# Kernel tuning notes

Hardware: AMD Instinct MI355X
Metric: run time of the kernel (lower is better)

Reference implementation:

```python
import jax, jax.numpy as jnp
import numpy as np

CDIM = 32
SCALES = (1, 16, 64, 256, 1024, 4096)  # last entry == T
INV_TEMP = 100.0
ENT_W = 0.1
COMMIT_W = 0.2
Q_SCALE = 1.0 / float(np.sqrt(CDIM))


def _interp_area(x, pt):
    # x: [B, T, C] -> [B, pt, C]; T divisible by pt so 'area' == block mean
    B, T, C = x.shape
    return x.reshape(B, pt, T // pt, C).mean(axis=2)


def _interp_linear(x, T):
    # x: [B, pt, C] -> [B, T, C]; mode='linear', align_corners=False
    pt = x.shape[1]
    pos = (jnp.arange(T, dtype=jnp.float32) + 0.5) * (pt / T) - 0.5
    pos = jnp.clip(pos, 0.0, pt - 1.0)
    lo = jnp.floor(pos).astype(jnp.int32)
    hi = jnp.minimum(lo + 1, pt - 1)
    w = (pos - lo.astype(jnp.float32))[None, :, None]
    return x[:, lo] * (1.0 - w) + x[:, hi] * w


def _bsq(f):
    # L2 normalize (torch F.normalize: clamp_min on norm)
    f = f / jnp.maximum(jnp.linalg.norm(f, axis=-1, keepdims=True), 1e-12)
    # sign quantize with STE
    zhat = jnp.where(f > 0, Q_SCALE, -Q_SCALE).astype(f.dtype)
    quantized = f + jax.lax.stop_gradient(zhat - f)
    # soft entropy loss
    p = jax.nn.sigmoid(-4.0 * f * (INV_TEMP / float(np.sqrt(CDIM))))
    prob = jnp.stack([p, 1.0 - p], axis=-1)  # [B, T, C, 2]
    ent = lambda c: -(c * jnp.log(c + 1e-8)).sum(axis=-1)
    per_sample_entropy = ent(prob).sum(axis=-1).mean()
    avg_prob = prob.mean(axis=(0, 1))  # [C, 2]
    cb_entropy = ent(avg_prob).sum()
    entropy_penalty = (per_sample_entropy - cb_entropy) / INV_TEMP
    commit = ((jax.lax.stop_gradient(quantized) - f) ** 2).sum(axis=-1).mean()
    aux = entropy_penalty * ENT_W + commit * COMMIT_W
    bits = (quantized > 0).astype(jnp.int32)
    return quantized, bits, aux


def setup_inputs() -> dict:
    key = jax.random.key(0)
    B, T, C = 128, SCALES[-1], CDIM
    return {"f_BTC": jax.random.normal(key, (B, T, C), dtype=jnp.float32)}


def reference(f_BTC):
    B, T, C = f_BTC.shape
    quantized_out = jnp.zeros_like(f_BTC)
    residual = f_BTC
    losses, bit_list = [], []
    for pt in SCALES:
        interp_res = _interp_area(residual, pt) if pt != T else residual
        q, bits, loss = _bsq(interp_res)
        q = _interp_linear(q, T) if pt != T else q
        residual = residual - jax.lax.stop_gradient(q)
        quantized_out = quantized_out + q
        bit_list.append(bits)
        losses.append(loss)
    all_losses = jnp.stack(losses, axis=-1)       # [num_scales]
    all_bits = jnp.concatenate(bit_list, axis=1)  # [B, sum(SCALES), C]
    return quantized_out, all_bits, all_losses
```

## Files before the change

kernel.cpp:

```cpp
#include <hip/hip_runtime.h>
#include <hip/hip_bf16.h>
#include <cstddef>
#include <cstdint>

#define NB 128
#define NT 4096
#define NC 32
#define BITROWS 5457
#define QV_ROWS 1361
#define QOUT_ELEMS (NB*NT*NC)
#define BITS_ELEMS (NB*BITROWS*NC)

#define ACC_OFF  22298624
#define S16_OFF  22302720

__device__ __constant__ float kQSC = 0.17677669529663687f;
__device__ __constant__ float kSIG = 17.67766952966369f;

__device__ __forceinline__ float interp_eval(const float* __restrict__ q, int P, int t, int c) {
  float pos = ((float)t + 0.5f) * ((float)P * (1.0f / 4096.0f)) - 0.5f;
  pos = fminf(fmaxf(pos, 0.0f), (float)(P - 1));
  const int lo = (int)pos;
  const int hi = min(lo + 1, P - 1);
  const float w = pos - (float)lo;
  const float a = __fmul_rn(q[lo * NC + c], 1.0f - w);
  const float b = __fmul_rn(q[hi * NC + c], w);
  return __fadd_rn(a, b);
}

__device__ __forceinline__ float interp_slice(const float* __restrict__ q, int P, int base, int t, int c) {
  float pos = ((float)t + 0.5f) * ((float)P * (1.0f / 4096.0f)) - 0.5f;
  pos = fminf(fmaxf(pos, 0.0f), (float)(P - 1));
  const int lo = (int)pos;
  const int hi = min(lo + 1, P - 1);
  const float w = pos - (float)lo;
  const float a = __fmul_rn(q[(lo - base) * NC + c], 1.0f - w);
  const float b = __fmul_rn(q[(hi - base) * NC + c], w);
  return __fadd_rn(a, b);
}

__device__ __forceinline__ void process_elem(
    float msum, float invn, int b, int rowOff, int j, int c,
    float* qlsRow, float* __restrict__ qvG, float* __restrict__ bitsG,
    float& entA, float& comA, float& pA)
{
  const float m = msum * invn;
  float ss = m * m;
  #pragma unroll
  for (int mk = 16; mk; mk >>= 1) ss += __shfl_xor(ss, mk, 32);
  const float den = fmaxf(sqrtf(ss), 1e-12f);
  const float fn = m / den;
  const bool bit = fn > 0.0f;
  const float zh = bit ? kQSC : -kQSC;
  const float qvv = fn + (zh - fn);
  if (qlsRow) qlsRow[c] = qvv;
  if (qvG) qvG[(size_t)b * (QV_ROWS * NC) + (size_t)(rowOff + j) * NC + c] = qvv;
  bitsG[(size_t)b * (BITROWS * NC) + (size_t)(rowOff + j) * NC + c] = bit ? 1.0f : 0.0f;
  const float arg = (-4.0f * fn) * kSIG;
  const float p = 1.0f / (1.0f + __expf(-arg));
  const float ent = -(p * __logf(p + 1e-8f) + (1.0f - p) * __logf((1.0f - p) + 1e-8f));
  const float d = qvv - fn;
  entA += ent; comA += d * d; pA += p;
}

__device__ __forceinline__ void reduce_losses(
    int sIdx, float entA, float comA, float pA, int tid, int nWaves,
    double* __restrict__ acc, float* redE, float* redC, float* redP)
{
  float e = entA, cm = comA;
  #pragma unroll
  for (int mk = 32; mk; mk >>= 1) { e += __shfl_xor(e, mk, 64); cm += __shfl_xor(cm, mk, 64); }
  const float p = pA + __shfl_xor(pA, 32, 64);
  const int w = tid >> 6, lane = tid & 63;
  if (lane == 0) { redE[w] = e; redC[w] = cm; }
  if (lane < 32) redP[w * 32 + lane] = p;
  __syncthreads();
  if (tid == 0) {
    double te = 0.0, tc = 0.0;
    for (int i = 0; i < nWaves; ++i) { te += (double)redE[i]; tc += (double)redC[i]; }
    atomicAdd(&acc[sIdx], te);
    atomicAdd(&acc[6 + sIdx], tc);
  }
  if (tid < 32) {
    float tp = 0.0f;
    for (int i = 0; i < nWaves; ++i) tp += redP[i * 32 + tid];
    atomicAdd(&acc[12 + sIdx * 32 + tid], (double)tp);
  }
  __syncthreads();
}

__global__ __launch_bounds__(256) void k_sum16(const float* __restrict__ f, float* __restrict__ S16) {
  const int idx = blockIdx.x * 256 + threadIdx.x;
  if (idx >= NB * 256 * NC) return;
  const int c = idx & 31;
  const int j = (idx >> 5) & 255;
  const int b = idx >> 13;
  const float* p = f + (size_t)b * (NT * NC) + (size_t)j * 16 * NC + c;
  float s = 0.0f;
  #pragma unroll
  for (int k = 0; k < 16; ++k) s += p[k * NC];
  S16[idx] = s;
}

__global__ __launch_bounds__(1024) void k_s0(
    const float* __restrict__ S16g, float* __restrict__ qv,
    float* __restrict__ bitsOut, double* __restrict__ acc)
{
  __shared__ float red[1024];
  __shared__ float redE[16], redC[16], redP[16 * 32];
  const int b = blockIdx.x, tid = threadIdx.x, c = tid & 31;
  const float* __restrict__ sb = S16g + (size_t)b * 8192;
  {
    const int g = tid >> 5;
    float part = 0.0f;
    #pragma unroll
    for (int j = 0; j < 8; ++j) part += sb[(size_t)(g * 8 + j) * NC + c];
    red[tid] = part;
  }
  __syncthreads();
  float entA = 0.0f, comA = 0.0f, pA = 0.0f;
  if (tid < 32) {
    float msum = 0.0f;
    for (int g = 0; g < 32; ++g) msum += red[g * 32 + tid];
    process_elem(msum, 1.0f / 4096.0f, b, 0, 0, tid, nullptr, qv, bitsOut, entA, comA, pA);
  }
  reduce_losses(0, entA, comA, pA, tid, 16, acc, redE, redC, redP);
}

__global__ __launch_bounds__(1024) void k_coarse2(
    const float* __restrict__ S16g,
    float* __restrict__ qv, float* __restrict__ bitsOut, double* __restrict__ acc)
{
  __shared__ float S[144 * NC];
  __shared__ float q1s[10 * NC];
  __shared__ float q2s[34 * NC];
  __shared__ float redE[16], redC[16], redP[16 * 32];
  const int b = blockIdx.x >> 1, seg = blockIdx.x & 1;
  const int tid = threadIdx.x, c = tid & 31;
  const int start = seg * 112;
  const int base1 = 8 * seg - 1, base2 = 32 * seg - 1;
  const float* __restrict__ sb = S16g + (size_t)b * 8192;
  const float* __restrict__ qb = qv + (size_t)b * (QV_ROWS * NC);

  for (int e = tid; e < 144 * NC; e += 1024)
    S[e] = sb[(size_t)(start + (e >> 5)) * NC + (e & 31)];
  __syncthreads();

  const float corr = 16.0f * qb[c];
  for (int e = tid; e < 144 * NC; e += 1024) S[e] -= corr;
  __syncthreads();

  float entA, comA, pA;

  entA = comA = pA = 0.0f;
  if (tid < 256) {
    const int jl = tid >> 5;
    const int j = 8 * seg + jl;
    float msum = 0.0f;
    for (int jj = 0; jj < 16; ++jj) msum += S[(j * 16 + jj - start) * NC + c];
    process_elem(msum, 1.0f / 256.0f, b, 1, j, c, &q1s[(j - base1) * NC], qv, bitsOut, entA, comA, pA);
  } else if (tid < 288) {
    const int jh = seg ? 7 : 8;
    float msum = 0.0f;
    for (int jj = 0; jj < 16; ++jj) msum += S[(jh * 16 + jj - start) * NC + c];
    const float m = msum * (1.0f / 256.0f);
    float ss = m * m;
    #pragma unroll
    for (int mk = 16; mk; mk >>= 1) ss += __shfl_xor(ss, mk, 32);
    const float den = fmaxf(sqrtf(ss), 1e-12f);
    const float fn = m / den;
    const float zh = (fn > 0.0f) ? kQSC : -kQSC;
    q1s[(jh - base1) * NC + c] = fn + (zh - fn);
  }
  reduce_losses(1, entA, comA, pA, tid, 16, acc, redE, redC, redP);

  {
    const int gc0 = seg ? 124 : 0;
    for (int e = tid; e < 132 * NC; e += 1024) {
      const int g = gc0 + (e >> 5);
      float cs = 0.0f;
      #pragma unroll
      for (int k = 0; k < 16; ++k) cs += interp_slice(q1s, 16, base1, g * 16 + k, c);
      S[(g - start) * NC + c] -= cs;
    }
  }
  __syncthreads();

  entA = comA = pA = 0.0f;
  {
    const int j2 = 32 * seg + (tid >> 5);
    float msum = 0.0f;
    #pragma unroll
    for (int jj = 0; jj < 4; ++jj) msum += S[(j2 * 4 + jj - start) * NC + c];
    process_elem(msum, 1.0f / 64.0f, b, 17, j2, c, &q2s[(j2 - base2) * NC], qv, bitsOut, entA, comA, pA);
  }
  if (tid < 32) {
    const int j2h = seg ? 31 : 32;
    float msum = 0.0f;
    #pragma unroll
    for (int jj = 0; jj < 4; ++jj) msum += S[(j2h * 4 + jj - start) * NC + c];
    const float m = msum * (1.0f / 64.0f);
    float ss = m * m;
    #pragma unroll
    for (int mk = 16; mk; mk >>= 1) ss += __shfl_xor(ss, mk, 32);
    const float den = fmaxf(sqrtf(ss), 1e-12f);
    const float fn = m / den;
    const float zh = (fn > 0.0f) ? kQSC : -kQSC;
    q2s[(j2h - base2) * NC + c] = fn + (zh - fn);
  }
  reduce_losses(2, entA, comA, pA, tid, 16, acc, redE, redC, redP);

  for (int e = tid; e < 128 * NC; e += 1024) {
    const int g = 128 * seg + (e >> 5);
    float cs = 0.0f;
    #pragma unroll
    for (int k = 0; k < 16; ++k) cs += interp_slice(q2s, 64, base2, g * 16 + k, c);
    S[(g - start) * NC + c] -= cs;
  }
  __syncthreads();

  entA = comA = pA = 0.0f;
  for (int out = tid; out < 128 * NC; out += 1024) {
    const int g = 128 * seg + (out >> 5);
    process_elem(S[(g - start) * NC + c], 1.0f / 16.0f, b, 81, g, c, nullptr, qv, bitsOut, entA, comA, pA);
  }
  reduce_losses(3, entA, comA, pA, tid, 16, acc, redE, redC, redP);
}

__global__ __launch_bounds__(256) void k_s45(
    const float* __restrict__ f, const float* __restrict__ qv,
    float* __restrict__ qout, float* __restrict__ bitsOut, double* __restrict__ acc)
{
  __shared__ float ql0[NC];
  __shared__ float ql1[3 * NC];
  __shared__ float ql2[6 * NC];
  __shared__ float ql3[18 * NC];
  __shared__ float ql4[66 * NC];
  __shared__ float redE[4], redC[4], redP[4 * 32];
  const int b = blockIdx.x >> 4, seg = blockIdx.x & 15;
  const int tid = threadIdx.x, c = tid & 31, rloc = tid >> 5;
  const int t0 = seg * 256;
  const float* __restrict__ qb = qv + (size_t)b * (QV_ROWS * NC);
  const float* __restrict__ fb = f + (size_t)b * (NT * NC);
  const int b1 = seg - 1, b2 = 4 * seg - 1, b3 = 16 * seg - 1, b4 = 64 * seg - 1;
  if (tid < NC) ql0[tid] = qb[tid];
  for (int e = tid; e < 3 * NC; e += 256) {
    const int r = min(max(b1 + (e >> 5), 0), 15);
    ql1[e] = qb[(1 + r) * NC + (e & 31)];
  }
  for (int e = tid; e < 6 * NC; e += 256) {
    const int r = min(max(b2 + (e >> 5), 0), 63);
    ql2[e] = qb[(17 + r) * NC + (e & 31)];
  }
  for (int e = tid; e < 18 * NC; e += 256) {
    const int r = min(max(b3 + (e >> 5), 0), 255);
    ql3[e] = qb[(81 + r) * NC + (e & 31)];
  }
  __syncthreads();

  float entA = 0.0f, comA = 0.0f, pA = 0.0f;
  for (int pass = 0; pass < 8; ++pass) {
    const int i = seg * 64 + pass * 8 + rloc;
    const float* fp = fb + (size_t)i * 4 * NC + c;
    float msum = 0.0f;
    #pragma unroll
    for (int k = 0; k < 4; ++k) {
      const int t = i * 4 + k;
      float r = fp[k * NC];
      r -= ql0[c];
      r -= interp_slice(ql1, 16,  b1, t, c);
      r -= interp_slice(ql2, 64,  b2, t, c);
      r -= interp_slice(ql3, 256, b3, t, c);
      msum += r;
    }
    process_elem(msum, 0.25f, b, 337, i, c,
                 &ql4[(size_t)(i - b4) * NC], nullptr, bitsOut, entA, comA, pA);
  }
  {
    int hr = -1;
    if (rloc == 0 && seg > 0)       hr = 64 * seg - 1;
    else if (rloc == 1 && seg < 15) hr = 64 * seg + 64;
    if (hr >= 0) {
      const float* fp = fb + (size_t)hr * 4 * NC + c;
      float msum = 0.0f;
      #pragma unroll
      for (int k = 0; k < 4; ++k) {
        const int t = hr * 4 + k;
        float r = fp[k * NC];
        r -= ql0[c];
        r -= interp_slice(ql1, 16,  b1, t, c);
        r -= interp_slice(ql2, 64,  b2, t, c);
        r -= interp_slice(ql3, 256, b3, t, c);
        msum += r;
      }
      const float m = msum * 0.25f;
      float ss = m * m;
      #pragma unroll
      for (int mk = 16; mk; mk >>= 1) ss += __shfl_xor(ss, mk, 32);
      const float den = fmaxf(sqrtf(ss), 1e-12f);
      const float fn = m / den;
      const float zh = (fn > 0.0f) ? kQSC : -kQSC;
      ql4[(size_t)(hr - b4) * NC + c] = fn + (zh - fn);
    }
  }
  reduce_losses(4, entA, comA, pA, tid, 4, acc, redE, redC, redP);

  entA = 0.0f; comA = 0.0f; pA = 0.0f;
  for (int pass = 0; pass < 32; ++pass) {
    const int t = t0 + pass * 8 + rloc;
    const float fv = fb[(size_t)t * NC + c];
    const float q0 = ql0[c];
    const float q1 = interp_slice(ql1, 16,   b1, t, c);
    const float q2 = interp_slice(ql2, 64,   b2, t, c);
    const float q3 = interp_slice(ql3, 256,  b3, t, c);
    const float q4 = interp_slice(ql4, 1024, b4, t, c);
    float r = fv;
    r -= q0; r -= q1; r -= q2; r -= q3; r -= q4;
    float qs = q0; qs += q1; qs += q2; qs += q3; qs += q4;
    float ss = r * r;
    #pragma unroll
    for (int mk = 16; mk; mk >>= 1) ss += __shfl_xor(ss, mk, 32);
    const float den = fmaxf(sqrtf(ss), 1e-12f);
    const float fn = r / den;
    const bool bit = fn > 0.0f;
    const float zh = bit ? kQSC : -kQSC;
    const float qvv = fn + (zh - fn);
    qout[(size_t)b * (NT * NC) + (size_t)t * NC + c] = qs + qvv;
    bitsOut[(size_t)b * (BITROWS * NC) + (size_t)(1361 + t) * NC + c] = bit ? 1.0f : 0.0f;
    const float arg = (-4.0f * fn) * kSIG;
    const float p = 1.0f / (1.0f + __expf(-arg));
    entA += -(p * __logf(p + 1e-8f) + (1.0f - p) * __logf((1.0f - p) + 1e-8f));
    const float d = qvv - fn;
    comA += d * d;
    pA += p;
  }
  reduce_losses(5, entA, comA, pA, tid, 4, acc, redE, redC, redP);
}

__global__ void k_losses(const double* __restrict__ acc, float* __restrict__ out) {
  const int s = threadIdx.x;
  if (s >= 6) return;
  const int pts[6] = {1, 16, 64, 256, 1024, 4096};
  const double n = 128.0 * (double)pts[s];
  const double pse = acc[s] / n;
  const double commit = acc[6 + s] / n;
  double cbe = 0.0;
  for (int c = 0; c < 32; ++c) {
    const double ap = acc[12 + s * 32 + c] / n;
    cbe += -(ap * log(ap + 1e-8) + (1.0 - ap) * log((1.0 - ap) + 1e-8));
  }
  const double pen = (pse - cbe) / 100.0;
  out[s] = (float)(pen * 0.1 + commit * 0.2);
}

extern "C" void kernel_launch(void* const* d_in, const int* in_sizes, int n_in,
                              void* d_out, int out_size, void* d_ws, size_t ws_size,
                              hipStream_t stream) {
  const float* f = (const float*)d_in[0];
  float* qout = (float*)d_out;
  float* bitsOut = qout + QOUT_ELEMS;
  float* lossesOut = qout + (QOUT_ELEMS + BITS_ELEMS);
  float* qv = (float*)d_ws;
  double* acc = (double*)((char*)d_ws + ACC_OFF);
  float* S16 = (float*)((char*)d_ws + S16_OFF);

  hipMemsetAsync(acc, 0, 204 * sizeof(double), stream);
  k_sum16<<<4096, 256, 0, stream>>>(f, S16);
  k_s0<<<NB, 1024, 0, stream>>>(S16, qv, bitsOut, acc);
  k_coarse2<<<NB * 2, 1024, 0, stream>>>(S16, qv, bitsOut, acc);
  k_s45<<<NB * 16, 256, 0, stream>>>(f, qv, qout, bitsOut, acc);
  k_losses<<<1, 64, 0, stream>>>(acc, lossesOut);
}
```

Baseline: 335.0 us.

## Keep stage-4 residuals in registers and reuse them for stage 5

```diff
diff --git a/kernel.cpp b/kernel.cpp
--- a/kernel.cpp
+++ b/kernel.cpp
@@ -227,7 +227,7 @@
   reduce_losses(3, entA, comA, pA, tid, 16, acc, redE, redC, redP);
 }
 
-__global__ __launch_bounds__(256) void k_s45(
+__global__ __launch_bounds__(1024) void k_s45(
     const float* __restrict__ f, const float* __restrict__ qv,
     float* __restrict__ qout, float* __restrict__ bitsOut, double* __restrict__ acc)
 {
@@ -236,41 +236,47 @@
   __shared__ float ql2[6 * NC];
   __shared__ float ql3[18 * NC];
   __shared__ float ql4[66 * NC];
-  __shared__ float redE[4], redC[4], redP[4 * 32];
+  __shared__ float redE[16], redC[16], redP[16 * 32];
   const int b = blockIdx.x >> 4, seg = blockIdx.x & 15;
   const int tid = threadIdx.x, c = tid & 31, rloc = tid >> 5;
-  const int t0 = seg * 256;
   const float* __restrict__ qb = qv + (size_t)b * (QV_ROWS * NC);
   const float* __restrict__ fb = f + (size_t)b * (NT * NC);
   const int b1 = seg - 1, b2 = 4 * seg - 1, b3 = 16 * seg - 1, b4 = 64 * seg - 1;
   if (tid < NC) ql0[tid] = qb[tid];
-  for (int e = tid; e < 3 * NC; e += 256) {
-    const int r = min(max(b1 + (e >> 5), 0), 15);
-    ql1[e] = qb[(1 + r) * NC + (e & 31)];
-  }
-  for (int e = tid; e < 6 * NC; e += 256) {
-    const int r = min(max(b2 + (e >> 5), 0), 63);
-    ql2[e] = qb[(17 + r) * NC + (e & 31)];
-  }
-  for (int e = tid; e < 18 * NC; e += 256) {
-    const int r = min(max(b3 + (e >> 5), 0), 255);
-    ql3[e] = qb[(81 + r) * NC + (e & 31)];
-  }
-  __syncthreads();
+  if (tid < 3 * NC) {
+    const int r = min(max(b1 + (tid >> 5), 0), 15);
+    ql1[tid] = qb[(1 + r) * NC + (tid & 31)];
+  }
+  if (tid < 6 * NC) {
+    const int r = min(max(b2 + (tid >> 5), 0), 63);
+    ql2[tid] = qb[(17 + r) * NC + (tid & 31)];
+  }
+  if (tid < 18 * NC) {
+    const int r = min(max(b3 + (tid >> 5), 0), 255);
+    ql3[tid] = qb[(81 + r) * NC + (tid & 31)];
+  }
+  __syncthreads();
+
+  float rA[2][4], qsA[2][4];
 
   float entA = 0.0f, comA = 0.0f, pA = 0.0f;
-  for (int pass = 0; pass < 8; ++pass) {
-    const int i = seg * 64 + pass * 8 + rloc;
+  #pragma unroll
+  for (int pass = 0; pass < 2; ++pass) {
+    const int i = seg * 64 + pass * 32 + rloc;
     const float* fp = fb + (size_t)i * 4 * NC + c;
     float msum = 0.0f;
     #pragma unroll
     for (int k = 0; k < 4; ++k) {
       const int t = i * 4 + k;
+      const float q0 = ql0[c];
+      const float q1 = interp_slice(ql1, 16,  b1, t, c);
+      const float q2 = interp_slice(ql2, 64,  b2, t, c);
+      const float q3 = interp_slice(ql3, 256, b3, t, c);
       float r = fp[k * NC];
-      r -= ql0[c];
-      r -= interp_slice(ql1, 16,  b1, t, c);
-      r -= interp_slice(ql2, 64,  b2, t, c);
-      r -= interp_slice(ql3, 256, b3, t, c);
+      r -= q0; r -= q1; r -= q2; r -= q3;
+      float qs = q0; qs += q1; qs += q2; qs += q3;
+      rA[pass][k] = r;
+      qsA[pass][k] = qs;
       msum += r;
     }
     process_elem(msum, 0.25f, b, 337, i, c,
@@ -303,38 +309,39 @@
       ql4[(size_t)(hr - b4) * NC + c] = fn + (zh - fn);
     }
   }
-  reduce_losses(4, entA, comA, pA, tid, 4, acc, redE, redC, redP);
+  reduce_losses(4, entA, comA, pA, tid, 16, acc, redE, redC, redP);
 
   entA = 0.0f; comA = 0.0f; pA = 0.0f;
-  for (int pass = 0; pass < 32; ++pass) {
-    const int t = t0 + pass * 8 + rloc;
-    const float fv = fb[(size_t)t * NC + c];
-    const float q0 = ql0[c];
-    const float q1 = interp_slice(ql1, 16,   b1, t, c);
-    const float q2 = interp_slice(ql2, 64,   b2, t, c);
-    const float q3 = interp_slice(ql3, 256,  b3, t, c);
-    const float q4 = interp_slice(ql4, 1024, b4, t, c);
-    float r = fv;
-    r -= q0; r -= q1; r -= q2; r -= q3; r -= q4;
-    float qs = q0; qs += q1; qs += q2; qs += q3; qs += q4;
-    float ss = r * r;
-    #pragma unroll
-    for (int mk = 16; mk; mk >>= 1) ss += __shfl_xor(ss, mk, 32);
-    const float den = fmaxf(sqrtf(ss), 1e-12f);
-    const float fn = r / den;
-    const bool bit = fn > 0.0f;
-    const float zh = bit ? kQSC : -kQSC;
-    const float qvv = fn + (zh - fn);
-    qout[(size_t)b * (NT * NC) + (size_t)t * NC + c] = qs + qvv;
-    bitsOut[(size_t)b * (BITROWS * NC) + (size_t)(1361 + t) * NC + c] = bit ? 1.0f : 0.0f;
-    const float arg = (-4.0f * fn) * kSIG;
-    const float p = 1.0f / (1.0f + __expf(-arg));
-    entA += -(p * __logf(p + 1e-8f) + (1.0f - p) * __logf((1.0f - p) + 1e-8f));
-    const float d = qvv - fn;
-    comA += d * d;
-    pA += p;
-  }
-  reduce_losses(5, entA, comA, pA, tid, 4, acc, redE, redC, redP);
+  #pragma unroll
+  for (int pass = 0; pass < 2; ++pass) {
+    const int i = seg * 64 + pass * 32 + rloc;
+    #pragma unroll
+    for (int k = 0; k < 4; ++k) {
+      const int t = i * 4 + k;
+      const float q4 = interp_slice(ql4, 1024, b4, t, c);
+      float r = rA[pass][k];
+      r -= q4;
+      float qs = qsA[pass][k];
+      qs += q4;
+      float ss = r * r;
+      #pragma unroll
+      for (int mk = 16; mk; mk >>= 1) ss += __shfl_xor(ss, mk, 32);
+      const float den = fmaxf(sqrtf(ss), 1e-12f);
+      const float fn = r / den;
+      const bool bit = fn > 0.0f;
+      const float zh = bit ? kQSC : -kQSC;
+      const float qvv = fn + (zh - fn);
+      qout[(size_t)b * (NT * NC) + (size_t)t * NC + c] = qs + qvv;
+      bitsOut[(size_t)b * (BITROWS * NC) + (size_t)(1361 + t) * NC + c] = bit ? 1.0f : 0.0f;
+      const float arg = (-4.0f * fn) * kSIG;
+      const float p = 1.0f / (1.0f + __expf(-arg));
+      entA += -(p * __logf(p + 1e-8f) + (1.0f - p) * __logf((1.0f - p) + 1e-8f));
+      const float d = qvv - fn;
+      comA += d * d;
+      pA += p;
+    }
+  }
+  reduce_losses(5, entA, comA, pA, tid, 16, acc, redE, redC, redP);
 }
 
 __global__ void k_losses(const double* __restrict__ acc, float* __restrict__ out) {
@@ -368,6 +375,6 @@
   k_sum16<<<4096, 256, 0, stream>>>(f, S16);
   k_s0<<<NB, 1024, 0, stream>>>(S16, qv, bitsOut, acc);
   k_coarse2<<<NB * 2, 1024, 0, stream>>>(S16, qv, bitsOut, acc);
-  k_s45<<<NB * 16, 256, 0, stream>>>(f, qv, qout, bitsOut, acc);
+  k_s45<<<NB * 16, 1024, 0, stream>>>(f, qv, qout, bitsOut, acc);
   k_losses<<<1, 64, 0, stream>>>(acc, lossesOut);
 }
```

Result: slower. 343.0 us (+2.4%).

## Fuse scale-4 and scale-5 passes with register-held residuals and pipelining

Applied to the files above, without the earlier changes.

```diff
diff --git a/kernel.cpp b/kernel.cpp
--- a/kernel.cpp
+++ b/kernel.cpp
@@ -239,7 +239,6 @@
   __shared__ float redE[4], redC[4], redP[4 * 32];
   const int b = blockIdx.x >> 4, seg = blockIdx.x & 15;
   const int tid = threadIdx.x, c = tid & 31, rloc = tid >> 5;
-  const int t0 = seg * 256;
   const float* __restrict__ qb = qv + (size_t)b * (QV_ROWS * NC);
   const float* __restrict__ fb = f + (size_t)b * (NT * NC);
   const int b1 = seg - 1, b2 = 4 * seg - 1, b3 = 16 * seg - 1, b4 = 64 * seg - 1;
@@ -258,14 +257,36 @@
   }
   __syncthreads();
 
-  float entA = 0.0f, comA = 0.0f, pA = 0.0f;
-  for (int pass = 0; pass < 8; ++pass) {
-    const int i = seg * 64 + pass * 8 + rloc;
+  float entA4 = 0.0f, comA4 = 0.0f, pA4 = 0.0f;
+  float entB = 0.0f, comB = 0.0f, pB = 0.0f;
+
+  auto do_A = [&](int p, float rc[4], float qc[4]) {
+    const int i = seg * 64 + p * 8 + rloc;
     const float* fp = fb + (size_t)i * 4 * NC + c;
     float msum = 0.0f;
     #pragma unroll
     for (int k = 0; k < 4; ++k) {
       const int t = i * 4 + k;
+      const float q0 = ql0[c];
+      const float q1 = interp_slice(ql1, 16,  b1, t, c);
+      const float q2 = interp_slice(ql2, 64,  b2, t, c);
+      const float q3 = interp_slice(ql3, 256, b3, t, c);
+      float r = fp[k * NC];
+      r -= q0; r -= q1; r -= q2; r -= q3;
+      float qs = q0; qs += q1; qs += q2; qs += q3;
+      rc[k] = r; qc[k] = qs;
+      msum += r;
+    }
+    process_elem(msum, 0.25f, b, 337, i, c,
+                 &ql4[(size_t)(i - b4) * NC], nullptr, bitsOut, entA4, comA4, pA4);
+  };
+
+  auto do_halo = [&](int hr) {
+    const float* fp = fb + (size_t)hr * 4 * NC + c;
+    float msum = 0.0f;
+    #pragma unroll
+    for (int k = 0; k < 4; ++k) {
+      const int t = hr * 4 + k;
       float r = fp[k * NC];
       r -= ql0[c];
       r -= interp_slice(ql1, 16,  b1, t, c);
@@ -273,68 +294,64 @@
       r -= interp_slice(ql3, 256, b3, t, c);
       msum += r;
     }
-    process_elem(msum, 0.25f, b, 337, i, c,
-                 &ql4[(size_t)(i - b4) * NC], nullptr, bitsOut, entA, comA, pA);
-  }
-  {
-    int hr = -1;
-    if (rloc == 0 && seg > 0)       hr = 64 * seg - 1;
-    else if (rloc == 1 && seg < 15) hr = 64 * seg + 64;
-    if (hr >= 0) {
-      const float* fp = fb + (size_t)hr * 4 * NC + c;
-      float msum = 0.0f;
-      #pragma unroll
-      for (int k = 0; k < 4; ++k) {
-        const int t = hr * 4 + k;
-        float r = fp[k * NC];
-        r -= ql0[c];
-        r -= interp_slice(ql1, 16,  b1, t, c);
-        r -= interp_slice(ql2, 64,  b2, t, c);
-        r -= interp_slice(ql3, 256, b3, t, c);
-        msum += r;
-      }
-      const float m = msum * 0.25f;
-      float ss = m * m;
+    const float m = msum * 0.25f;
+    float ss = m * m;
+    #pragma unroll
+    for (int mk = 16; mk; mk >>= 1) ss += __shfl_xor(ss, mk, 32);
+    const float den = fmaxf(sqrtf(ss), 1e-12f);
+    const float fn = m / den;
+    const float zh = (fn > 0.0f) ? kQSC : -kQSC;
+    ql4[(size_t)(hr - b4) * NC + c] = fn + (zh - fn);
+  };
+
+  auto do_B = [&](int p, const float rc[4], const float qc[4]) {
+    const int i = seg * 64 + p * 8 + rloc;
+    #pragma unroll
+    for (int k = 0; k < 4; ++k) {
+      const int t = i * 4 + k;
+      const float q4 = interp_slice(ql4, 1024, b4, t, c);
+      float r = rc[k];
+      r -= q4;
+      float qs = qc[k];
+      qs += q4;
+      float ss = r * r;
       #pragma unroll
       for (int mk = 16; mk; mk >>= 1) ss += __shfl_xor(ss, mk, 32);
       const float den = fmaxf(sqrtf(ss), 1e-12f);
-      const float fn = m / den;
-      const float zh = (fn > 0.0f) ? kQSC : -kQSC;
-      ql4[(size_t)(hr - b4) * NC + c] = fn + (zh - fn);
+      const float fn = r / den;
+      const bool bit = fn > 0.0f;
+      const float zh = bit ? kQSC : -kQSC;
+      const float qvv = fn + (zh - fn);
+      qout[(size_t)b * (NT * NC) + (size_t)t * NC + c] = qs + qvv;
+      bitsOut[(size_t)b * (BITROWS * NC) + (size_t)(1361 + t) * NC + c] = bit ? 1.0f : 0.0f;
+      const float arg = (-4.0f * fn) * kSIG;
+      const float p2 = 1.0f / (1.0f + __expf(-arg));
+      entB += -(p2 * __logf(p2 + 1e-8f) + (1.0f - p2) * __logf((1.0f - p2) + 1e-8f));
+      const float d = qvv - fn;
+      comB += d * d;
+      pB += p2;
     }
-  }
-  reduce_losses(4, entA, comA, pA, tid, 4, acc, redE, redC, redP);
-
-  entA = 0.0f; comA = 0.0f; pA = 0.0f;
-  for (int pass = 0; pass < 32; ++pass) {
-    const int t = t0 + pass * 8 + rloc;
-    const float fv = fb[(size_t)t * NC + c];
-    const float q0 = ql0[c];
-    const float q1 = interp_slice(ql1, 16,   b1, t, c);
-    const float q2 = interp_slice(ql2, 64,   b2, t, c);
-    const float q3 = interp_slice(ql3, 256,  b3, t, c);
-    const float q4 = interp_slice(ql4, 1024, b4, t, c);
-    float r = fv;
-    r -= q0; r -= q1; r -= q2; r -= q3; r -= q4;
-    float qs = q0; qs += q1; qs += q2; qs += q3; qs += q4;
-    float ss = r * r;
-    #pragma unroll
-    for (int mk = 16; mk; mk >>= 1) ss += __shfl_xor(ss, mk, 32);
-    const float den = fmaxf(sqrtf(ss), 1e-12f);
-    const float fn = r / den;
-    const bool bit = fn > 0.0f;
-    const float zh = bit ? kQSC : -kQSC;
-    const float qvv = fn + (zh - fn);
-    qout[(size_t)b * (NT * NC) + (size_t)t * NC + c] = qs + qvv;
-    bitsOut[(size_t)b * (BITROWS * NC) + (size_t)(1361 + t) * NC + c] = bit ? 1.0f : 0.0f;
-    const float arg = (-4.0f * fn) * kSIG;
-    const float p = 1.0f / (1.0f + __expf(-arg));
-    entA += -(p * __logf(p + 1e-8f) + (1.0f - p) * __logf((1.0f - p) + 1e-8f));
-    const float d = qvv - fn;
-    comA += d * d;
-    pA += p;
-  }
-  reduce_losses(5, entA, comA, pA, tid, 4, acc, redE, redC, redP);
+  };
+
+  float rAp[4], qsAp[4];
+  float rAc[4], qsAc[4];
+
+  do_A(0, rAp, qsAp);
+  if (rloc == 0 && seg > 0) do_halo(64 * seg - 1);
+
+  for (int p = 1; p < 8; ++p) {
+    do_A(p, rAc, qsAc);
+    __syncthreads();
+    do_B(p - 1, rAp, qsAp);
+    #pragma unroll
+    for (int k = 0; k < 4; ++k) { rAp[k] = rAc[k]; qsAp[k] = qsAc[k]; }
+  }
+  if (rloc == 1 && seg < 15) do_halo(64 * seg + 64);
+  __syncthreads();
+  do_B(7, rAp, qsAp);
+
+  reduce_losses(4, entA4, comA4, pA4, tid, 4, acc, redE, redC, redP);
+  reduce_losses(5, entB, comB, pB, tid, 4, acc, redE, redC, redP);
 }
 
 __global__ void k_losses(const double* __restrict__ acc, float* __restrict__ out) {
```

Result: faster. 320.6 us (-4.3%).
